# Optimization experiments

Hardware: AMD Instinct MI355X
Metric: run time of the kernel (lower is better)

## Reference

```python
import jax, jax.numpy as jnp
import numpy as np
from jax import lax

EPS = 1e-5
S_CENTROIDS = 2048
K_NEIGH = 32


def _fps(xyz, S):
    """Farthest point sampling. xyz: (B,N,3) -> idx (B,S) int32."""
    B, N, _ = xyz.shape

    def body(carry, _):
        dist, farthest = carry  # (B,N), (B,)
        centroid = jnp.take_along_axis(xyz, farthest[:, None, None], axis=1)  # (B,1,3)
        d = jnp.sum((xyz - centroid) ** 2, axis=-1)  # (B,N)
        dist = jnp.minimum(dist, d)
        nxt = jnp.argmax(dist, axis=-1).astype(jnp.int32)
        return (dist, nxt), farthest

    init = (jnp.full((B, N), 1e10, xyz.dtype), jnp.zeros((B,), jnp.int32))
    _, idx = lax.scan(body, init, None, length=S)
    return idx.T  # (B,S)


def _knn(q, p, K):
    """q: (B,S,3) queries, p: (B,N,3) points -> idx (B,S,K) of K nearest."""
    d = (jnp.sum(q * q, -1)[:, :, None] + jnp.sum(p * p, -1)[:, None, :]
         - 2.0 * jnp.einsum('bsd,bnd->bsn', q, p))  # (B,S,N) sq dists
    _, idx = lax.top_k(-d, K)
    return idx


def _mlp_layer(x, w, g, b, m, v):
    # x: (B,S,K,Cin); 1x1 conv == channel matmul, then eval-mode BN, then ReLU
    x = jnp.einsum('bskc,oc->bsko', x, w)
    x = (x - m) * (g * lax.rsqrt(v + EPS)) + b
    return jax.nn.relu(x)


def setup_inputs() -> dict:
    key = jax.random.key(0)
    ks = jax.random.split(key, 8)
    B, N, D = 4, 8192, 64
    inp = {
        'xyz': jax.random.normal(ks[0], (B, N, 3), jnp.float32),
        'points': jax.random.normal(ks[1], (B, D, N), jnp.float32),
        'w0': jax.random.normal(ks[2], (64, 67), jnp.float32) * (1.0 / np.sqrt(67)),
        'g0': jnp.ones((64,), jnp.float32), 'b0': jnp.zeros((64,), jnp.float32),
        'm0': jnp.zeros((64,), jnp.float32), 'v0': jnp.ones((64,), jnp.float32),
        'w1': jax.random.normal(ks[3], (64, 64), jnp.float32) * (1.0 / np.sqrt(64)),
        'g1': jnp.ones((64,), jnp.float32), 'b1': jnp.zeros((64,), jnp.float32),
        'm1': jnp.zeros((64,), jnp.float32), 'v1': jnp.ones((64,), jnp.float32),
        'w2': jax.random.normal(ks[4], (128, 64), jnp.float32) * (1.0 / np.sqrt(64)),
        'g2': jnp.ones((128,), jnp.float32), 'b2': jnp.zeros((128,), jnp.float32),
        'm2': jnp.zeros((128,), jnp.float32), 'v2': jnp.ones((128,), jnp.float32),
    }
    return inp


def reference(xyz, points, w0, g0, b0, m0, v0, w1, g1, b1, m1, v1,
              w2, g2, b2, m2, v2):
    B, N, _ = xyz.shape
    S, K = S_CENTROIDS, K_NEIGH

    # FPS centroids (S < N path of the module)
    fps_idx = _fps(xyz, S)                                        # (B,S)
    new_xyz = jnp.take_along_axis(xyz, fps_idx[..., None], axis=1)  # (B,S,3)

    # KNN grouping
    idx = _knn(new_xyz, xyz, K)                                   # (B,S,K)
    grouped_xyz = jnp.take_along_axis(xyz[:, None], idx[..., None], axis=2)  # (B,S,K,3)
    grouped_xyz = grouped_xyz - new_xyz[:, :, None, :]

    # gather neighbor features: points (B,D,N) -> (B,N,D) -> (B,S,K,D)
    pts = jnp.transpose(points, (0, 2, 1))
    neigh = jnp.take_along_axis(pts[:, None], idx[..., None], axis=2)
    grouped = jnp.concatenate([grouped_xyz, neigh], axis=-1)      # (B,S,K,3+D)

    x = _mlp_layer(grouped, w0, g0, b0, m0, v0)
    x = _mlp_layer(x, w1, g1, b1, m1, v1)
    x = _mlp_layer(x, w2, g2, b2, m2, v2)                         # (B,S,K,128)

    new_points = jnp.transpose(jnp.max(x, axis=2), (0, 2, 1))     # (B,128,S)
    return new_xyz, new_points
```

## Files before the change

kernel.cpp:

```cpp
#include <hip/hip_runtime.h>
#include <cfloat>
#include <climits>

#define NPTS   8192
#define SCENT  2048
#define KNEIGH 32
#define BATCH  4
#define DFEAT  64
#define FPS_T  512
#define NV     8
#define NW     8
#define CAP    64
#define NCONS  252
#define CPB    63

typedef float v2f __attribute__((ext_vector_type(2)));

#define DPPMAX(u, ctrl, rmask)                                                        \
    { unsigned _t = (unsigned)__builtin_amdgcn_update_dpp(0, (int)(u), (ctrl),        \
                                                          (rmask), 0xf, false);      \
      (u) = ((u) > _t) ? (u) : _t; }

struct FpsSh {
    float sx[NPTS], sy[NPTS], sz[NPTS];
    float hx[SCENT], hy[SCENT], hz[SCENT];
    alignas(16) unsigned slotV[2][NW];
    alignas(16) unsigned slotM[2][NW];
    int scand[CAP];
    int scnt;
    alignas(8) double sdd[2][NW];
    double sfv[NW];
    int sfo[NW];
};
struct KnnSh {
    float  spx[2048], spy[2048], spz[2048];
    double sp2[2048];
    float  tile[32 * 33];
};
union ShU { FpsSh f; KnnSh k; };

__global__ __launch_bounds__(FPS_T, 1) void fused_kernel(
        const float* __restrict__ xyz, float* __restrict__ new_xyz,
        const float* __restrict__ pts, float* __restrict__ ptsT,
        int* __restrict__ knn_idx, int* __restrict__ progress) {
    __shared__ ShU sh;
    const int t = threadIdx.x;
    const int lane = t & 63, w = t >> 6;

    if (blockIdx.x < BATCH) {
        FpsSh& S = sh.f;
        const int b = blockIdx.x;
        const float* X = xyz + (size_t)b * NPTS * 3;

        for (int p = t; p < NPTS; p += FPS_T) {
            S.sx[p] = X[3 * p + 0]; S.sy[p] = X[3 * p + 1]; S.sz[p] = X[3 * p + 2];
        }

        v2f px2[NV], py2[NV], pz2[NV], dist2[NV];
#pragma unroll
        for (int j = 0; j < NV; ++j) {
            int pA = t + FPS_T * j, pB = t + FPS_T * (j + NV);
            px2[j] = (v2f){X[3 * pA + 0], X[3 * pB + 0]};
            py2[j] = (v2f){X[3 * pA + 1], X[3 * pB + 1]};
            pz2[j] = (v2f){X[3 * pA + 2], X[3 * pB + 2]};
            dist2[j] = (v2f){1e10f, 1e10f};
        }
        float cx = X[0], cy = X[1], cz = X[2];
        int buf = 0;
        __syncthreads();

#pragma unroll 1
        for (int s = 0; s < SCENT; ++s) {
            if (t == 0) { S.hx[s] = cx; S.hy[s] = cy; S.hz[s] = cz; }

            const v2f cxx = {cx, cx}, cyy = {cy, cy}, czz = {cz, cz};
            v2f m2 = {-1.f, -1.f}, s2 = {-1.f, -1.f};
#pragma unroll
            for (int j = 0; j < NV; ++j) {
                v2f dx = px2[j] - cxx;
                v2f dy = py2[j] - cyy;
                v2f dz = pz2[j] - czz;
                v2f d  = __builtin_elementwise_fma(dx, dx,
                         __builtin_elementwise_fma(dy, dy, dz * dz));
                v2f nd = __builtin_elementwise_min(dist2[j], d);
                dist2[j] = nd;
                v2f lo = __builtin_elementwise_min(m2, nd);
                s2 = __builtin_elementwise_max(s2, lo);
                m2 = __builtin_elementwise_max(m2, nd);
            }
            const float m   = fmaxf(m2.x, m2.y);
            const float sec = fmaxf(fmaxf(s2.x, s2.y), fminf(m2.x, m2.y));

            int mi = 0;
#pragma unroll
            for (int j = 0; j < NV; ++j) {
                mi = (dist2[j].x == m) ? (t + FPS_T * j)        : mi;
                mi = (dist2[j].y == m) ? (t + FPS_T * (j + NV)) : mi;
            }

            unsigned myU = __float_as_uint(m);
            unsigned u = myU;
            DPPMAX(u, 0x111, 0xf);
            DPPMAX(u, 0x112, 0xf);
            DPPMAX(u, 0x114, 0xf);
            DPPMAX(u, 0x118, 0xf);
            DPPMAX(u, 0x142, 0xa);
            DPPMAX(u, 0x143, 0xc);
            const unsigned wu = (unsigned)__builtin_amdgcn_readlane((int)u, 63);

            unsigned long long wb = __ballot(myU == wu);
            const int wl   = __ffsll(wb) - 1;
            const int widx = __builtin_amdgcn_readlane(mi, wl);
            const float thwf = __fmul_rn(__uint_as_float(wu), 0.999998f);
            unsigned long long b1m = __ballot(m >= thwf);
            unsigned long long b2m = __ballot(sec >= thwf);
            const unsigned tw = (b2m || __popcll(b1m) >= 2) ? 1u : 0u;
            if (lane == 0) {
                S.slotV[buf][w] = wu;
                S.slotM[buf][w] = (unsigned)widx | (tw << 14);
            }
            __syncthreads();

            unsigned sv[NW], sm[NW];
            {
                const uint4* vp = (const uint4*)&S.slotV[buf][0];
                const uint4* mp = (const uint4*)&S.slotM[buf][0];
                uint4 a = vp[0], c = vp[1], e = mp[0], f = mp[1];
                sv[0] = a.x; sv[1] = a.y; sv[2] = a.z; sv[3] = a.w;
                sv[4] = c.x; sv[5] = c.y; sv[6] = c.z; sv[7] = c.w;
                sm[0] = e.x; sm[1] = e.y; sm[2] = e.z; sm[3] = e.w;
                sm[4] = f.x; sm[5] = f.y; sm[6] = f.z; sm[7] = f.w;
            }
            unsigned gu = sv[0];
#pragma unroll
            for (int k = 1; k < NW; ++k) gu = (sv[k] > gu) ? sv[k] : gu;
            const float gvf  = __uint_as_float(gu);
            const float gthf = __fmul_rn(gvf, 0.999998f);
            const unsigned ugth = __float_as_uint(gthf);
            int nw = 0; unsigned meta = 0;
#pragma unroll
            for (int k = NW - 1; k >= 0; --k) {
                nw += (sv[k] >= ugth) ? 1 : 0;
                meta = (sv[k] == gu) ? sm[k] : meta;
            }
            const int wtie = (meta >> 14) & 1;
            int i1 = (int)(meta & 0x3fffu);

            if (nw >= 2 || wtie) {
                if (t == 0) S.scnt = 0;
                __syncthreads();
#pragma unroll
                for (int j = 0; j < NV; ++j) {
                    if (dist2[j].x >= gthf) {
                        int slot = atomicAdd(&S.scnt, 1);
                        if (slot < CAP) S.scand[slot] = t + FPS_T * j;
                    }
                    if (dist2[j].y >= gthf) {
                        int slot = atomicAdd(&S.scnt, 1);
                        if (slot < CAP) S.scand[slot] = t + FPS_T * (j + NV);
                    }
                }
                __syncthreads();
                const int mm = S.scnt;
                if (mm <= CAP) {
                    double bd = -1.0; int bi = INT_MAX;
#pragma unroll 1
                    for (int k = 0; k < mm; ++k) {
                        const int pos = S.scand[k];
                        const double pxd = (double)S.sx[pos], pyd = (double)S.sy[pos],
                                     pzd = (double)S.sz[pos];
                        double dd = 1e10;
                        for (int i = t; i <= s; i += FPS_T) {
                            double ddx = __dsub_rn(pxd, (double)S.hx[i]);
                            double ddy = __dsub_rn(pyd, (double)S.hy[i]);
                            double ddz = __dsub_rn(pzd, (double)S.hz[i]);
                            double d = __dadd_rn(__dadd_rn(__dmul_rn(ddx, ddx), __dmul_rn(ddy, ddy)),
                                                 __dmul_rn(ddz, ddz));
                            dd = fmin(dd, d);
                        }
#pragma unroll
                        for (int off = 32; off >= 1; off >>= 1)
                            dd = fmin(dd, __shfl_down(dd, off));
                        if (lane == 0) S.sdd[k & 1][w] = dd;
                        __syncthreads();
                        double ddm = S.sdd[k & 1][0];
#pragma unroll
                        for (int w2 = 1; w2 < NW; ++w2) ddm = fmin(ddm, S.sdd[k & 1][w2]);
                        if (ddm > bd || (ddm == bd && pos < bi)) { bd = ddm; bi = pos; }
                    }
                    i1 = bi;
                } else {
                    double bv = -1.0; int bi = INT_MAX;
#pragma unroll 1
                    for (int j = 0; j < 2 * NV; ++j) {
                        const int jj = j & (NV - 1);
                        const bool hiHalf = j >= NV;
                        const double pxd = (double)(hiHalf ? px2[jj].y : px2[jj].x);
                        const double pyd = (double)(hiHalf ? py2[jj].y : py2[jj].x);
                        const double pzd = (double)(hiHalf ? pz2[jj].y : pz2[jj].x);
                        double dd = 1e10;
                        for (int i = 0; i <= s; ++i) {
                            double ddx = __dsub_rn(pxd, (double)S.hx[i]);
                            double ddy = __dsub_rn(pyd, (double)S.hy[i]);
                            double ddz = __dsub_rn(pzd, (double)S.hz[i]);
                            double d = __dadd_rn(__dadd_rn(__dmul_rn(ddx, ddx), __dmul_rn(ddy, ddy)),
                                                 __dmul_rn(ddz, ddz));
                            dd = fmin(dd, d);
                        }
                        int pidx = t + FPS_T * j;
                        if (dd > bv || (dd == bv && pidx < bi)) { bv = dd; bi = pidx; }
                    }
#pragma unroll
                    for (int off = 32; off >= 1; off >>= 1) {
                        double ov = __shfl_down(bv, off);
                        int    oi = __shfl_down(bi, off);
                        if (ov > bv || (ov == bv && oi < bi)) { bv = ov; bi = oi; }
                    }
                    if (lane == 0) { S.sfv[w] = bv; S.sfo[w] = bi; }
                    __syncthreads();
                    bv = S.sfv[0]; bi = S.sfo[0];
#pragma unroll
                    for (int w2 = 1; w2 < NW; ++w2) {
                        double ov = S.sfv[w2]; int oi = S.sfo[w2];
                        if (ov > bv || (ov == bv && oi < bi)) { bv = ov; bi = oi; }
                    }
                    i1 = bi;
                }
                __syncthreads();
            }
            cx = S.sx[i1]; cy = S.sy[i1]; cz = S.sz[i1];

            if ((s & 63) == 63) {
                const int base0 = s - 63;
                if (t < 64 * 3) {
                    int ci = base0 + t / 3;
                    int cmp = t - (t / 3) * 3;
                    float v = (cmp == 0) ? S.hx[ci] : ((cmp == 1) ? S.hy[ci] : S.hz[ci]);
                    __hip_atomic_store(&new_xyz[((size_t)b * SCENT + base0) * 3 + t], v,
                                       __ATOMIC_RELAXED, __HIP_MEMORY_SCOPE_AGENT);
                }
                __syncthreads();
                if (t == 0)
                    __hip_atomic_store(&progress[b], s + 1,
                                       __ATOMIC_RELEASE, __HIP_MEMORY_SCOPE_AGENT);
            }
            buf ^= 1;
        }
    } else {
        KnnSh& K = sh.k;
        const int local = blockIdx.x - BATCH;
        const int batch = local / CPB;
        const int cl    = local % CPB;
        const int tx = t & 31, ty = t >> 5;

        for (int tid2 = local; tid2 < 2048; tid2 += NCONS) {
            const int bt = tid2 >> 9, rest = tid2 & 511;
            const int d0 = (rest >> 8) * 32, n0 = (rest & 255) * 32;
            __syncthreads();
#pragma unroll
            for (int i = 0; i < 2; ++i)
                K.tile[(ty + 16 * i) * 33 + tx] =
                    pts[(size_t)bt * DFEAT * NPTS + (size_t)(d0 + ty + 16 * i) * NPTS + n0 + tx];
            __syncthreads();
#pragma unroll
            for (int i = 0; i < 2; ++i)
                ptsT[(size_t)bt * NPTS * DFEAT + (size_t)(n0 + ty + 16 * i) * DFEAT + d0 + tx] =
                    K.tile[tx * 33 + ty + 16 * i];
        }

        const float* Xb = xyz + (size_t)batch * NPTS * 3;
#pragma unroll 1
        for (int r = 0; ; ++r) {
            const int sBase = r * (CPB * NW) + cl * NW;
            if (sBase >= SCENT) break;
            const int sMax = min(sBase + NW - 1, SCENT - 1);
            if (t == 0) {
                while (__hip_atomic_load(&progress[batch], __ATOMIC_ACQUIRE,
                                         __HIP_MEMORY_SCOPE_AGENT) < sMax + 1)
                    __builtin_amdgcn_s_sleep(8);
            }
            __syncthreads();

            const int sQ = min(sBase + w, SCENT - 1);
            const float* q = new_xyz + ((size_t)batch * SCENT + sQ) * 3;
            const double qx = (double)q[0], qy = (double)q[1], qz = (double)q[2];
            const double q2 = __dadd_rn(__dadd_rn(__dmul_rn(qx, qx), __dmul_rn(qy, qy)),
                                        __dmul_rn(qz, qz));

            double ld   = DBL_MAX;
            int    li   = 0x7fffffff;
            double taud = DBL_MAX;
            int    taui = 0x7fffffff;

#pragma unroll 1
            for (int c = 0; c < 4; ++c) {
                __syncthreads();
#pragma unroll
                for (int r2 = 0; r2 < 4; ++r2) {
                    int pl = r2 * 512 + t;
                    int p  = c * 2048 + pl;
                    float x = Xb[3 * p + 0], y = Xb[3 * p + 1], z = Xb[3 * p + 2];
                    K.spx[pl] = x; K.spy[pl] = y; K.spz[pl] = z;
                    double dx = (double)x, dy = (double)y, dz = (double)z;
                    K.sp2[pl] = __dadd_rn(__dadd_rn(__dmul_rn(dx, dx), __dmul_rn(dy, dy)),
                                          __dmul_rn(dz, dz));
                }
                __syncthreads();
#pragma unroll 1
                for (int i = 0; i < 32; ++i) {
                    const int pl   = i * 64 + lane;
                    const int pidx = c * 2048 + pl;
                    double px = (double)K.spx[pl], py = (double)K.spy[pl],
                           pz = (double)K.spz[pl];
                    double qp = __dadd_rn(__dadd_rn(__dmul_rn(qx, px), __dmul_rn(qy, py)),
                                          __dmul_rn(qz, pz));
                    double d  = __dsub_rn(__dadd_rn(q2, K.sp2[pl]), __dmul_rn(2.0, qp));
                    bool cand = (d < taud) || (d == taud && pidx < taui);
                    unsigned long long mmask = __ballot(cand);
                    while (mmask) {
                        int sl = __ffsll((unsigned long long)mmask) - 1;
                        mmask &= mmask - 1;
                        double dv = __shfl(d, sl);
                        int    iv = __shfl(pidx, sl);
                        if (dv < taud || (dv == taud && iv < taui)) {
                            bool gt = (lane < 32) && (ld > dv || (ld == dv && li > iv));
                            unsigned long long gm = __ballot(gt);
                            double ud = __shfl_up(ld, 1);
                            int    ui = __shfl_up(li, 1);
                            if (gt) { ld = ud; li = ui; }
                            bool first = gt && ((lane == 0) || !((gm >> (lane - 1)) & 1ull));
                            if (first) { ld = dv; li = iv; }
                            taud = __shfl(ld, 31);
                            taui = __shfl(li, 31);
                        }
                    }
                }
            }
            if (sBase + w < SCENT && lane < 32)
                knn_idx[((size_t)batch * SCENT + sQ) * KNEIGH + lane] = li;
        }
    }
}

__global__ __launch_bounds__(256) void mlp_kernel(
    const float* __restrict__ xyz, const float* __restrict__ new_xyz,
    const float* __restrict__ ptsT, const int* __restrict__ knn_idx,
    const float* __restrict__ w0, const float* __restrict__ g0,
    const float* __restrict__ b0, const float* __restrict__ m0,
    const float* __restrict__ v0, const float* __restrict__ w1,
    const float* __restrict__ g1, const float* __restrict__ b1,
    const float* __restrict__ m1, const float* __restrict__ v1,
    const float* __restrict__ w2, const float* __restrict__ g2,
    const float* __restrict__ b2, const float* __restrict__ m2,
    const float* __restrict__ v2, float* __restrict__ out_points) {

    __shared__ float regA[8192];
    __shared__ float regB[4096];
    __shared__ float prm[512];

    const int t = threadIdx.x;
    if (t < 64) {
        float a0v = g0[t] / sqrtf(v0[t] + 1e-5f);
        prm[t]       = a0v;
        prm[64 + t]  = b0[t] - m0[t] * a0v;
        float a1v = g1[t] / sqrtf(v1[t] + 1e-5f);
        prm[128 + t] = a1v;
        prm[192 + t] = b1[t] - m1[t] * a1v;
    } else if (t < 192) {
        int o = t - 64;
        float a2v = g2[o] / sqrtf(v2[o] + 1e-5f);
        prm[256 + o] = a2v;
        prm[384 + o] = b2[o] - m2[o] * a2v;
    }
    for (int idx = t; idx < 64 * 68; idx += 256) {
        int o = idx / 68, i = idx - o * 68;
        float v;
        if (i < 64)      v = w0[o * 67 + 3 + i];
        else if (i < 67) v = w0[o * 67 + (i - 64)];
        else             v = 0.0f;
        regA[idx] = v;
    }
    for (int idx = t; idx < 64 * 64; idx += 256) regB[idx] = w1[idx];
    __syncthreads();

    const int gid = blockIdx.x * 256 + t;
    const int sl  = gid >> 5;
    const int s   = sl & (SCENT - 1);
    const int b   = sl >> 11;
    const int nidx = knn_idx[gid];

    const float* q  = new_xyz + (size_t)(b * SCENT + s) * 3;
    const float* P3 = xyz + (size_t)(b * NPTS + nidx) * 3;
    const float dx = P3[0] - q[0], dy = P3[1] - q[1], dz = P3[2] - q[2];

    const float4* F = (const float4*)(ptsT + ((size_t)b * NPTS + nidx) * 64);
    float4 xv[17];
#pragma unroll
    for (int i = 0; i < 16; ++i) xv[i] = F[i];
    xv[16] = make_float4(dx, dy, dz, 0.0f);

    float h0[64];
    const float4* W0 = (const float4*)regA;
#pragma unroll
    for (int o = 0; o < 64; ++o) {
        float acc = 0.f;
#pragma unroll
        for (int i = 0; i < 17; ++i) {
            float4 w = W0[o * 17 + i];
            acc = fmaf(xv[i].x, w.x, acc);
            acc = fmaf(xv[i].y, w.y, acc);
            acc = fmaf(xv[i].z, w.z, acc);
            acc = fmaf(xv[i].w, w.w, acc);
        }
        h0[o] = fmaxf(fmaf(acc, prm[o], prm[64 + o]), 0.f);
    }
    __syncthreads();
    for (int idx = t; idx < 128 * 64; idx += 256) regA[idx] = w2[idx];
    __syncthreads();

    float h1[64];
    const float4* W1 = (const float4*)regB;
#pragma unroll
    for (int o = 0; o < 64; ++o) {
        float acc = 0.f;
#pragma unroll
        for (int i = 0; i < 16; ++i) {
            float4 w = W1[o * 16 + i];
            acc = fmaf(h0[4 * i + 0], w.x, acc);
            acc = fmaf(h0[4 * i + 1], w.y, acc);
            acc = fmaf(h0[4 * i + 2], w.z, acc);
            acc = fmaf(h0[4 * i + 3], w.w, acc);
        }
        h1[o] = fmaxf(fmaf(acc, prm[128 + o], prm[192 + o]), 0.f);
    }

    const float4* W2 = (const float4*)regA;
    float* outp = out_points + (size_t)b * 128 * SCENT + s;
    const int lane = t & 63;
#pragma unroll 1
    for (int o = 0; o < 128; ++o) {
        float acc = 0.f;
#pragma unroll
        for (int i = 0; i < 16; ++i) {
            float4 w = W2[o * 16 + i];
            acc = fmaf(h1[4 * i + 0], w.x, acc);
            acc = fmaf(h1[4 * i + 1], w.y, acc);
            acc = fmaf(h1[4 * i + 2], w.z, acc);
            acc = fmaf(h1[4 * i + 3], w.w, acc);
        }
        float y = fmaxf(fmaf(acc, prm[256 + o], prm[384 + o]), 0.f);
#pragma unroll
        for (int off = 16; off >= 1; off >>= 1) y = fmaxf(y, __shfl_xor(y, off));
        if ((lane & 31) == 0) outp[(size_t)o * SCENT] = y;
    }
}

extern "C" void kernel_launch(void* const* d_in, const int* in_sizes, int n_in,
                              void* d_out, int out_size, void* d_ws, size_t ws_size,
                              hipStream_t stream) {
    const float* xyz    = (const float*)d_in[0];
    const float* points = (const float*)d_in[1];
    const float* w0 = (const float*)d_in[2];
    const float* g0 = (const float*)d_in[3];
    const float* b0 = (const float*)d_in[4];
    const float* m0 = (const float*)d_in[5];
    const float* v0 = (const float*)d_in[6];
    const float* w1 = (const float*)d_in[7];
    const float* g1 = (const float*)d_in[8];
    const float* b1 = (const float*)d_in[9];
    const float* m1 = (const float*)d_in[10];
    const float* v1 = (const float*)d_in[11];
    const float* w2 = (const float*)d_in[12];
    const float* g2 = (const float*)d_in[13];
    const float* b2 = (const float*)d_in[14];
    const float* m2 = (const float*)d_in[15];
    const float* v2 = (const float*)d_in[16];

    float* out_xyz    = (float*)d_out;
    float* out_points = (float*)d_out + (size_t)BATCH * SCENT * 3;

    char* ws = (char*)d_ws;
    int*   progress = (int*)ws;
    int*   knn_idx  = (int*)(ws + 32768);
    float* ptsT     = (float*)(ws + 32768 + (size_t)BATCH * SCENT * KNEIGH * 4);

    void* kargs[] = { (void*)&xyz, (void*)&out_xyz, (void*)&points,
                      (void*)&ptsT, (void*)&knn_idx, (void*)&progress };
    hipLaunchCooperativeKernel((const void*)fused_kernel,
                               dim3(BATCH + NCONS), dim3(FPS_T), kargs, 0, stream);

    mlp_kernel<<<(BATCH * SCENT * KNEIGH) / 256, 256, 0, stream>>>(
        xyz, out_xyz, ptsT, knn_idx,
        w0, g0, b0, m0, v0, w1, g1, b1, m1, v1, w2, g2, b2, m2, v2, out_points);
}
```

Before: 2.596 ms.

## Fuse MLP into KNN consumer blocks of the cooperative FPS kernel

Removes the separate MLP kernel launch and the global knn_idx round-trip. Each KNN consumer wave now runs the three-layer MLP and max-pool for its centroid right after computing the neighbours, so MLP work overlaps with the still-running sequential FPS producer blocks. A global counter makes sure the transposed feature buffer is complete before any block reads it, and the weights are preloaded into the consumers' shared memory. The cost is a much larger shared-memory footprint and heavy register pressure in the consumer blocks. The MLP also now runs on only 252 blocks instead of a full-width grid, which could slow it if the FPS stage does not hide it.

```diff
diff --git a/kernel.cpp b/kernel.cpp
--- a/kernel.cpp
+++ b/kernel.cpp
@@ -32,17 +32,30 @@
     double sfv[NW];
     int sfo[NW];
 };
-struct KnnSh {
+struct ConsSh {
     float  spx[2048], spy[2048], spz[2048];
     double sp2[2048];
     float  tile[32 * 33];
+    float  regA[64 * 68];
+    float  regB[64 * 64];
+    float  regC[128 * 64];
+    float  prm[512];
 };
-union ShU { FpsSh f; KnnSh k; };
+union ShU { FpsSh f; ConsSh c; };
 
 __global__ __launch_bounds__(FPS_T, 1) void fused_kernel(
         const float* __restrict__ xyz, float* __restrict__ new_xyz,
         const float* __restrict__ pts, float* __restrict__ ptsT,
-        int* __restrict__ knn_idx, int* __restrict__ progress) {
+        int* __restrict__ progress, int* __restrict__ tcount,
+        float* __restrict__ out_points,
+        const float* __restrict__ w0, const float* __restrict__ g0,
+        const float* __restrict__ b0, const float* __restrict__ m0,
+        const float* __restrict__ v0, const float* __restrict__ w1,
+        const float* __restrict__ g1, const float* __restrict__ b1,
+        const float* __restrict__ m1, const float* __restrict__ v1,
+        const float* __restrict__ w2, const float* __restrict__ g2,
+        const float* __restrict__ b2, const float* __restrict__ m2,
+        const float* __restrict__ v2) {
     __shared__ ShU sh;
     const int t = threadIdx.x;
     const int lane = t & 63, w = t >> 6;
@@ -185,7 +198,7 @@
                         __syncthreads();
                         double ddm = S.sdd[k & 1][0];
 #pragma unroll
-                        for (int w2 = 1; w2 < NW; ++w2) ddm = fmin(ddm, S.sdd[k & 1][w2]);
+                        for (int w2i = 1; w2i < NW; ++w2i) ddm = fmin(ddm, S.sdd[k & 1][w2i]);
                         if (ddm > bd || (ddm == bd && pos < bi)) { bd = ddm; bi = pos; }
                     }
                     i1 = bi;
@@ -220,8 +233,8 @@
                     __syncthreads();
                     bv = S.sfv[0]; bi = S.sfo[0];
 #pragma unroll
-                    for (int w2 = 1; w2 < NW; ++w2) {
-                        double ov = S.sfv[w2]; int oi = S.sfo[w2];
+                    for (int w2i = 1; w2i < NW; ++w2i) {
+                        double ov = S.sfv[w2i]; int oi = S.sfo[w2i];
                         if (ov > bv || (ov == bv && oi < bi)) { bv = ov; bi = oi; }
                     }
                     i1 = bi;
@@ -247,7 +260,7 @@
             buf ^= 1;
         }
     } else {
-        KnnSh& K = sh.k;
+        ConsSh& K = sh.c;
         const int local = blockIdx.x - BATCH;
         const int batch = local / CPB;
         const int cl    = local % CPB;
@@ -266,6 +279,34 @@
             for (int i = 0; i < 2; ++i)
                 ptsT[(size_t)bt * NPTS * DFEAT + (size_t)(n0 + ty + 16 * i) * DFEAT + d0 + tx] =
                     K.tile[tx * 33 + ty + 16 * i];
+        }
+        if (t == 0) {
+            __threadfence();
+            atomicAdd(tcount, 1);
+        }
+
+        for (int idx = t; idx < 64 * 68; idx += FPS_T) {
+            int o = idx / 68, i = idx - o * 68;
+            float v;
+            if (i < 64)      v = w0[o * 67 + 3 + i];
+            else if (i < 67) v = w0[o * 67 + (i - 64)];
+            else             v = 0.0f;
+            K.regA[idx] = v;
+        }
+        for (int idx = t; idx < 64 * 64; idx += FPS_T)  K.regB[idx] = w1[idx];
+        for (int idx = t; idx < 128 * 64; idx += FPS_T) K.regC[idx] = w2[idx];
+        if (t < 64) {
+            float a0v = g0[t] / sqrtf(v0[t] + 1e-5f);
+            K.prm[t]       = a0v;
+            K.prm[64 + t]  = b0[t] - m0[t] * a0v;
+            float a1v = g1[t] / sqrtf(v1[t] + 1e-5f);
+            K.prm[128 + t] = a1v;
+            K.prm[192 + t] = b1[t] - m1[t] * a1v;
+        } else if (t < 192) {
+            int o = t - 64;
+            float a2v = g2[o] / sqrtf(v2[o] + 1e-5f);
+            K.prm[256 + o] = a2v;
+            K.prm[384 + o] = b2[o] - m2[o] * a2v;
         }
 
         const float* Xb = xyz + (size_t)batch * NPTS * 3;
@@ -278,12 +319,18 @@
                 while (__hip_atomic_load(&progress[batch], __ATOMIC_ACQUIRE,
                                          __HIP_MEMORY_SCOPE_AGENT) < sMax + 1)
                     __builtin_amdgcn_s_sleep(8);
+                if (r == 0) {
+                    while (__hip_atomic_load(tcount, __ATOMIC_ACQUIRE,
+                                             __HIP_MEMORY_SCOPE_AGENT) < NCONS)
+                        __builtin_amdgcn_s_sleep(8);
+                }
             }
             __syncthreads();
 
             const int sQ = min(sBase + w, SCENT - 1);
             const float* q = new_xyz + ((size_t)batch * SCENT + sQ) * 3;
-            const double qx = (double)q[0], qy = (double)q[1], qz = (double)q[2];
+            const float qfx = q[0], qfy = q[1], qfz = q[2];
+            const double qx = (double)qfx, qy = (double)qfy, qz = (double)qfz;
             const double q2 = __dadd_rn(__dadd_rn(__dmul_rn(qx, qx), __dmul_rn(qy, qy)),
                                         __dmul_rn(qz, qz));
 
@@ -336,122 +383,69 @@
                     }
                 }
             }
-            if (sBase + w < SCENT && lane < 32)
-                knn_idx[((size_t)batch * SCENT + sQ) * KNEIGH + lane] = li;
-        }
-    }
-}
-
-__global__ __launch_bounds__(256) void mlp_kernel(
-    const float* __restrict__ xyz, const float* __restrict__ new_xyz,
-    const float* __restrict__ ptsT, const int* __restrict__ knn_idx,
-    const float* __restrict__ w0, const float* __restrict__ g0,
-    const float* __restrict__ b0, const float* __restrict__ m0,
-    const float* __restrict__ v0, const float* __restrict__ w1,
-    const float* __restrict__ g1, const float* __restrict__ b1,
-    const float* __restrict__ m1, const float* __restrict__ v1,
-    const float* __restrict__ w2, const float* __restrict__ g2,
-    const float* __restrict__ b2, const float* __restrict__ m2,
-    const float* __restrict__ v2, float* __restrict__ out_points) {
-
-    __shared__ float regA[8192];
-    __shared__ float regB[4096];
-    __shared__ float prm[512];
-
-    const int t = threadIdx.x;
-    if (t < 64) {
-        float a0v = g0[t] / sqrtf(v0[t] + 1e-5f);
-        prm[t]       = a0v;
-        prm[64 + t]  = b0[t] - m0[t] * a0v;
-        float a1v = g1[t] / sqrtf(v1[t] + 1e-5f);
-        prm[128 + t] = a1v;
-        prm[192 + t] = b1[t] - m1[t] * a1v;
-    } else if (t < 192) {
-        int o = t - 64;
-        float a2v = g2[o] / sqrtf(v2[o] + 1e-5f);
-        prm[256 + o] = a2v;
-        prm[384 + o] = b2[o] - m2[o] * a2v;
-    }
-    for (int idx = t; idx < 64 * 68; idx += 256) {
-        int o = idx / 68, i = idx - o * 68;
-        float v;
-        if (i < 64)      v = w0[o * 67 + 3 + i];
-        else if (i < 67) v = w0[o * 67 + (i - 64)];
-        else             v = 0.0f;
-        regA[idx] = v;
-    }
-    for (int idx = t; idx < 64 * 64; idx += 256) regB[idx] = w1[idx];
-    __syncthreads();
-
-    const int gid = blockIdx.x * 256 + t;
-    const int sl  = gid >> 5;
-    const int s   = sl & (SCENT - 1);
-    const int b   = sl >> 11;
-    const int nidx = knn_idx[gid];
-
-    const float* q  = new_xyz + (size_t)(b * SCENT + s) * 3;
-    const float* P3 = xyz + (size_t)(b * NPTS + nidx) * 3;
-    const float dx = P3[0] - q[0], dy = P3[1] - q[1], dz = P3[2] - q[2];
-
-    const float4* F = (const float4*)(ptsT + ((size_t)b * NPTS + nidx) * 64);
-    float4 xv[17];
-#pragma unroll
-    for (int i = 0; i < 16; ++i) xv[i] = F[i];
-    xv[16] = make_float4(dx, dy, dz, 0.0f);
-
-    float h0[64];
-    const float4* W0 = (const float4*)regA;
-#pragma unroll
-    for (int o = 0; o < 64; ++o) {
-        float acc = 0.f;
-#pragma unroll
-        for (int i = 0; i < 17; ++i) {
-            float4 w = W0[o * 17 + i];
-            acc = fmaf(xv[i].x, w.x, acc);
-            acc = fmaf(xv[i].y, w.y, acc);
-            acc = fmaf(xv[i].z, w.z, acc);
-            acc = fmaf(xv[i].w, w.w, acc);
-        }
-        h0[o] = fmaxf(fmaf(acc, prm[o], prm[64 + o]), 0.f);
-    }
-    __syncthreads();
-    for (int idx = t; idx < 128 * 64; idx += 256) regA[idx] = w2[idx];
-    __syncthreads();
-
-    float h1[64];
-    const float4* W1 = (const float4*)regB;
-#pragma unroll
-    for (int o = 0; o < 64; ++o) {
-        float acc = 0.f;
-#pragma unroll
-        for (int i = 0; i < 16; ++i) {
-            float4 w = W1[o * 16 + i];
-            acc = fmaf(h0[4 * i + 0], w.x, acc);
-            acc = fmaf(h0[4 * i + 1], w.y, acc);
-            acc = fmaf(h0[4 * i + 2], w.z, acc);
-            acc = fmaf(h0[4 * i + 3], w.w, acc);
-        }
-        h1[o] = fmaxf(fmaf(acc, prm[128 + o], prm[192 + o]), 0.f);
-    }
-
-    const float4* W2 = (const float4*)regA;
-    float* outp = out_points + (size_t)b * 128 * SCENT + s;
-    const int lane = t & 63;
-#pragma unroll 1
-    for (int o = 0; o < 128; ++o) {
-        float acc = 0.f;
-#pragma unroll
-        for (int i = 0; i < 16; ++i) {
-            float4 w = W2[o * 16 + i];
-            acc = fmaf(h1[4 * i + 0], w.x, acc);
-            acc = fmaf(h1[4 * i + 1], w.y, acc);
-            acc = fmaf(h1[4 * i + 2], w.z, acc);
-            acc = fmaf(h1[4 * i + 3], w.w, acc);
-        }
-        float y = fmaxf(fmaf(acc, prm[256 + o], prm[384 + o]), 0.f);
-#pragma unroll
-        for (int off = 16; off >= 1; off >>= 1) y = fmaxf(y, __shfl_xor(y, off));
-        if ((lane & 31) == 0) outp[(size_t)o * SCENT] = y;
+
+            if (sBase + w < SCENT && lane < 32) {
+                const int nidx = li;
+                const float* P3 = Xb + (size_t)nidx * 3;
+                const float dx = P3[0] - qfx, dy = P3[1] - qfy, dz = P3[2] - qfz;
+
+                const float4* F = (const float4*)(ptsT + ((size_t)batch * NPTS + nidx) * 64);
+                float4 xv[17];
+#pragma unroll
+                for (int i = 0; i < 16; ++i) xv[i] = F[i];
+                xv[16] = make_float4(dx, dy, dz, 0.0f);
+
+                float h0[64];
+                const float4* W0 = (const float4*)K.regA;
+#pragma unroll
+                for (int o = 0; o < 64; ++o) {
+                    float acc = 0.f;
+#pragma unroll
+                    for (int i = 0; i < 17; ++i) {
+                        float4 ww = W0[o * 17 + i];
+                        acc = fmaf(xv[i].x, ww.x, acc);
+                        acc = fmaf(xv[i].y, ww.y, acc);
+                        acc = fmaf(xv[i].z, ww.z, acc);
+                        acc = fmaf(xv[i].w, ww.w, acc);
+                    }
+                    h0[o] = fmaxf(fmaf(acc, K.prm[o], K.prm[64 + o]), 0.f);
+                }
+                float h1[64];
+                const float4* W1 = (const float4*)K.regB;
+#pragma unroll
+                for (int o = 0; o < 64; ++o) {
+                    float acc = 0.f;
+#pragma unroll
+                    for (int i = 0; i < 16; ++i) {
+                        float4 ww = W1[o * 16 + i];
+                        acc = fmaf(h0[4 * i + 0], ww.x, acc);
+                        acc = fmaf(h0[4 * i + 1], ww.y, acc);
+                        acc = fmaf(h0[4 * i + 2], ww.z, acc);
+                        acc = fmaf(h0[4 * i + 3], ww.w, acc);
+                    }
+                    h1[o] = fmaxf(fmaf(acc, K.prm[128 + o], K.prm[192 + o]), 0.f);
+                }
+                const float4* W2 = (const float4*)K.regC;
+                float* outp = out_points + (size_t)batch * 128 * SCENT + sQ;
+#pragma unroll 1
+                for (int o = 0; o < 128; ++o) {
+                    float acc = 0.f;
+#pragma unroll
+                    for (int i = 0; i < 16; ++i) {
+                        float4 ww = W2[o * 16 + i];
+                        acc = fmaf(h1[4 * i + 0], ww.x, acc);
+                        acc = fmaf(h1[4 * i + 1], ww.y, acc);
+                        acc = fmaf(h1[4 * i + 2], ww.z, acc);
+                        acc = fmaf(h1[4 * i + 3], ww.w, acc);
+                    }
+                    float y = fmaxf(fmaf(acc, K.prm[256 + o], K.prm[384 + o]), 0.f);
+#pragma unroll
+                    for (int off = 16; off >= 1; off >>= 1)
+                        y = fmaxf(y, __shfl_xor(y, off));
+                    if (lane == 0) outp[(size_t)o * SCENT] = y;
+                }
+            }
+        }
     }
 }
 
@@ -481,15 +475,16 @@
 
     char* ws = (char*)d_ws;
     int*   progress = (int*)ws;
-    int*   knn_idx  = (int*)(ws + 32768);
-    float* ptsT     = (float*)(ws + 32768 + (size_t)BATCH * SCENT * KNEIGH * 4);
-
-    void* kargs[] = { (void*)&xyz, (void*)&out_xyz, (void*)&points,
-                      (void*)&ptsT, (void*)&knn_idx, (void*)&progress };
+    int*   tcount   = (int*)(ws + 64);
+    float* ptsT     = (float*)(ws + 32768);
+
+    hipMemsetAsync(ws, 0, 128, stream);
+
+    void* kargs[] = { (void*)&xyz, (void*)&out_xyz, (void*)&points, (void*)&ptsT,
+                      (void*)&progress, (void*)&tcount, (void*)&out_points,
+                      (void*)&w0, (void*)&g0, (void*)&b0, (void*)&m0, (void*)&v0,
+                      (void*)&w1, (void*)&g1, (void*)&b1, (void*)&m1, (void*)&v1,
+                      (void*)&w2, (void*)&g2, (void*)&b2, (void*)&m2, (void*)&v2 };
     hipLaunchCooperativeKernel((const void*)fused_kernel,
                                dim3(BATCH + NCONS), dim3(FPS_T), kargs, 0, stream);
-
-    mlp_kernel<<<(BATCH * SCENT * KNEIGH) / 256, 256, 0, stream>>>(
-        xyz, out_xyz, ptsT, knn_idx,
-        w0, g0, b0, m0, v0, w1, g1, b1, m1, v1, w2, g2, b2, m2, v2, out_points);
 }
```

Result: faster. 2.486 ms (-4.3%).
